# Kernel optimization log

Measured on AMD Instinct MI355X. Metric: run time of the kernel, lower is better.

## Reference

```python
import jax, jax.numpy as jnp
import numpy as np

N = 524288   # number of 2D query points
HID = 100    # hidden width (layers = [2, 100, 1])


def setup_inputs() -> dict:
    key = jax.random.key(0)
    k0, k1, k2, k3 = jax.random.split(key, 4)
    f = jax.random.normal(k0, (N, 1), dtype=jnp.float32)   # unused (overwritten in torch fwd)
    xy = jax.random.normal(k1, (N, 2), dtype=jnp.float32)
    # MLP params: Linear(2->100), tanh, Linear(100->1)
    W1 = jax.random.normal(k2, (2, HID), dtype=jnp.float32) * (1.0 / np.sqrt(2.0))
    b1 = jnp.zeros((HID,), dtype=jnp.float32)
    W2 = jax.random.normal(k3, (HID, 1), dtype=jnp.float32) * (1.0 / np.sqrt(HID))
    b2 = jnp.zeros((1,), dtype=jnp.float32)
    return {"f": f, "xy": xy, "W1": W1, "b1": b1, "W2": W2, "b2": b2}


def reference(f, xy, W1, b1, W2, b2):
    # f = MLP(xy) = W2^T tanh(xy W1 + b1) + b2  (scalar per point)
    # The torch module computes the 2x2 Hessian of f via nested autograd.grad.
    # For a single-hidden-layer tanh MLP the Hessian is analytic:
    #   a = xy W1 + b1; h = tanh(a); tanh'' = -2 h (1 - h^2)
    #   H_kl = sum_j W2_j * tanh''(a_j) * W1_kj * W1_lj
    a = xy @ W1 + b1                      # [N, HID]
    h = jnp.tanh(a)
    coef = (-2.0 * h * (1.0 - h * h)) * W2[:, 0]   # [N, HID]
    w1x, w1y = W1[0], W1[1]               # [HID] each
    Hxx = coef @ (w1x * w1x)              # [N] = d2f/dxdx
    Hxy = coef @ (w1x * w1y)              # [N] = d2f/dxdy
    Hyy = coef @ (w1y * w1y)              # [N] = d2f/dydy
    u = Hxy - Hyy
    v = Hxy - Hxx
    return jnp.stack([u, v], axis=-1)     # [N, 2]
```

## Files before the change

### kernel.cpp

```cpp
#include <hip/hip_runtime.h>

#define NPTS 524288
#define HID 100
#define BLK 256

typedef float v2f __attribute__((ext_vector_type(2)));

#if __has_builtin(__builtin_elementwise_fma)
#define VFMA(a, b, c) __builtin_elementwise_fma((a), (b), (c))
#else
#define VFMA(a, b, c) ((a) * (b) + (c))
#endif

__global__ void __launch_bounds__(BLK)
kDivFree_main(const float2* __restrict__ xy,
              const float* __restrict__ W1,
              const float* __restrict__ b1,
              const float* __restrict__ W2,
              float2* __restrict__ out) {
    __shared__ float4 sA[HID];
    __shared__ float  sKv[HID];

    int t = threadIdx.x;
    if (t < HID) {
        const float C = 2.8853900817779268f;
        float w1x = W1[t], w1y = W1[HID + t], w2 = W2[t];
        sA[t] = make_float4(w1x * C, w1y * C, b1[t] * C,
                            2.0f * w2 * w1y * (w1x - w1y));
        sKv[t] = 2.0f * w2 * w1x * (w1y - w1x);
    }
    __syncthreads();

    const float4* sK4 = (const float4*)sKv;

    int base = blockIdx.x * (BLK * 2) + threadIdx.x;
    float2 p0 = xy[base];
    float2 p1 = xy[base + BLK];
    v2f px = {p0.x, p1.x};
    v2f py = {p0.y, p1.y};
    v2f u = {0.0f, 0.0f};
    v2f v = {0.0f, 0.0f};
    const v2f one = 1.0f, mtwo = -2.0f, mone = -1.0f;

#pragma unroll 5
    for (int j4 = 0; j4 < HID / 4; ++j4) {
        float4 K = sK4[j4];
        float kva[4] = {K.x, K.y, K.z, K.w};
#pragma unroll
        for (int jj = 0; jj < 4; ++jj) {
            float4 A = sA[j4 * 4 + jj];
            v2f ax = A.x, ay = A.y, az = A.z, ku = A.w, kv = kva[jj];
            v2f y = VFMA(px, ax, VFMA(py, ay, az));
            v2f e;
            e.x = __builtin_amdgcn_exp2f(y.x);
            e.y = __builtin_amdgcn_exp2f(y.y);
            v2f d = e + one;
            v2f r;
            r.x = __builtin_amdgcn_rcpf(d.x);
            r.y = __builtin_amdgcn_rcpf(d.y);
            v2f h  = VFMA(mtwo, r, one);
            v2f hm = VFMA(h, h, mone);
            v2f s  = h * hm;
            u = VFMA(s, ku, u);
            v = VFMA(s, kv, v);
        }
    }

    out[base]       = make_float2(u.x, v.x);
    out[base + BLK] = make_float2(u.y, v.y);
}

extern "C" void kernel_launch(void* const* d_in, const int* in_sizes, int n_in,
                              void* d_out, int out_size, void* d_ws, size_t ws_size,
                              hipStream_t stream) {
    const float* xy = (const float*)d_in[1];
    const float* W1 = (const float*)d_in[2];
    const float* b1 = (const float*)d_in[3];
    const float* W2 = (const float*)d_in[4];

    kDivFree_main<<<NPTS / (BLK * 2), BLK, 0, stream>>>(
        (const float2*)xy, W1, b1, W2, (float2*)d_out);
}
```

Measured before the change: 19.73 us.

## Precompute weight tables in a prep kernel and read them via scalar loads

Moves the per-block weight preprocessing into a separate single-block prep kernel that writes the packed coefficient tables to workspace. The main kernel drops its shared-memory staging and __syncthreads, and reads the tables through pointers made wave-uniform with readfirstlane, so the compiler can use scalar (SMEM) loads instead of LDS reads. This removes the LDS traffic and the barrier but adds a second kernel launch and its dependency.

```diff
diff --git a/kernel.cpp b/kernel.cpp
--- a/kernel.cpp
+++ b/kernel.cpp
@@ -12,26 +12,35 @@
 #define VFMA(a, b, c) ((a) * (b) + (c))
 #endif
 
+__global__ void kDivFree_prep(const float* __restrict__ W1,
+                              const float* __restrict__ b1,
+                              const float* __restrict__ W2,
+                              float4* __restrict__ tabA,
+                              float*  __restrict__ tabK) {
+    int j = threadIdx.x;
+    if (j < HID) {
+        const float C = 2.8853900817779268f;
+        float w1x = W1[j], w1y = W1[HID + j], w2 = W2[j];
+        tabA[j] = make_float4(w1x * C, w1y * C, b1[j] * C,
+                              2.0f * w2 * w1y * (w1x - w1y));
+        tabK[j] = 2.0f * w2 * w1x * (w1y - w1x);
+    }
+}
+
+__device__ __forceinline__ const float4* uniform_ptr(const float4* p) {
+    uint64_t u = (uint64_t)p;
+    uint32_t lo = __builtin_amdgcn_readfirstlane((uint32_t)u);
+    uint32_t hi = __builtin_amdgcn_readfirstlane((uint32_t)(u >> 32));
+    return (const float4*)(((uint64_t)hi << 32) | (uint64_t)lo);
+}
+
 __global__ void __launch_bounds__(BLK)
 kDivFree_main(const float2* __restrict__ xy,
-              const float* __restrict__ W1,
-              const float* __restrict__ b1,
-              const float* __restrict__ W2,
+              const float4* __restrict__ tabA_,
+              const float4* __restrict__ tabK_,
               float2* __restrict__ out) {
-    __shared__ float4 sA[HID];
-    __shared__ float  sKv[HID];
-
-    int t = threadIdx.x;
-    if (t < HID) {
-        const float C = 2.8853900817779268f;
-        float w1x = W1[t], w1y = W1[HID + t], w2 = W2[t];
-        sA[t] = make_float4(w1x * C, w1y * C, b1[t] * C,
-                            2.0f * w2 * w1y * (w1x - w1y));
-        sKv[t] = 2.0f * w2 * w1x * (w1y - w1x);
-    }
-    __syncthreads();
-
-    const float4* sK4 = (const float4*)sKv;
+    const float4* tabA = uniform_ptr(tabA_);
+    const float4* tabK = uniform_ptr(tabK_);
 
     int base = blockIdx.x * (BLK * 2) + threadIdx.x;
     float2 p0 = xy[base];
@@ -44,11 +53,11 @@
 
 #pragma unroll 5
     for (int j4 = 0; j4 < HID / 4; ++j4) {
-        float4 K = sK4[j4];
+        float4 K = tabK[j4];
         float kva[4] = {K.x, K.y, K.z, K.w};
 #pragma unroll
         for (int jj = 0; jj < 4; ++jj) {
-            float4 A = sA[j4 * 4 + jj];
+            float4 A = tabA[j4 * 4 + jj];
             v2f ax = A.x, ay = A.y, az = A.z, ku = A.w, kv = kva[jj];
             v2f y = VFMA(px, ax, VFMA(py, ay, az));
             v2f e;
@@ -77,7 +86,10 @@
     const float* W1 = (const float*)d_in[2];
     const float* b1 = (const float*)d_in[3];
     const float* W2 = (const float*)d_in[4];
+    float4* tabA = (float4*)d_ws;
+    float*  tabK = (float*)((char*)d_ws + 1600);
 
+    kDivFree_prep<<<1, 128, 0, stream>>>(W1, b1, W2, tabA, tabK);
     kDivFree_main<<<NPTS / (BLK * 2), BLK, 0, stream>>>(
-        (const float2*)xy, W1, b1, W2, (float2*)d_out);
+        (const float2*)xy, tabA, (const float4*)tabK, (float2*)d_out);
 }
```

After: 25.41 us. 1.29x slower.
